# Kernel tuning notes

Measured on AMD Instinct MI355X. Metric: run time of the kernel, lower is better.

Reference implementation:

```python
import jax, jax.numpy as jnp
import numpy as np

N = 8192      # nodes
D = 256       # feature dim
GAMMA = 10.0
EPS = 1e-6
DIAG_FILL = -1e-6
# std = 0 in DGM.__init__ default -> the normal(mean=0, std=0) noise is exactly zero, so it is omitted.


def _embed(x, W, edges):
    # minimal message-passing embed_f: h = relu(xW + sum_{(s,d) in E} (xW)[s] -> d)
    h = x @ W
    agg = jax.ops.segment_sum(h[edges[0]], edges[1], num_segments=N)
    return jax.nn.relu(h + agg)


def _cdist(x):
    # pairwise euclidean distance, [N, N]
    sq = jnp.sum(x * x, axis=-1)
    d2 = sq[:, None] + sq[None, :] - 2.0 * (x @ x.T)
    return jnp.sqrt(jnp.clip(d2, 0.0))


def _layernorm(z, gamma, beta):
    # scalar-affine LayerNorm with unbiased std (torch x.std default ddof=1)
    mean = jnp.mean(z, axis=-1, keepdims=True)
    std = jnp.std(z, axis=-1, ddof=1, keepdims=True)
    return gamma * (z - mean) / (std + EPS) + beta


def _entmax15(z):
    # 1.5-entmax over last axis (Peters et al. 2019, exact sort-based algorithm)
    z = z / 2.0
    z = z - jnp.max(z, axis=-1, keepdims=True)
    zs = -jnp.sort(-z, axis=-1)                      # descending sort per row
    k = jnp.arange(1, z.shape[-1] + 1, dtype=z.dtype)
    mean = jnp.cumsum(zs, axis=-1) / k
    meansq = jnp.cumsum(zs * zs, axis=-1) / k
    ss = k * (meansq - mean * mean)
    delta = (1.0 - ss) / k
    tau = mean - jnp.sqrt(jnp.clip(delta, 0.0))
    support = jnp.sum(tau <= zs, axis=-1)            # support size per row
    tau_star = jnp.take_along_axis(tau, (support - 1)[..., None], axis=-1)
    p = jnp.clip(z - tau_star, 0.0)
    return p * p


def setup_inputs() -> dict:
    key = jax.random.key(0)
    k1, k2, k3 = jax.random.split(key, 3)
    x = jax.random.normal(k1, (N, D), dtype=jnp.float32)
    edges = jax.random.randint(k2, (2, 262144), 0, N)
    W = jax.random.normal(k3, (D, D), dtype=jnp.float32) * (1.0 / np.sqrt(D))
    gamma = jnp.full((1,), GAMMA, dtype=jnp.float32)
    beta = jnp.zeros((1,), dtype=jnp.float32)
    return {"x": x, "W": W, "gamma": gamma, "beta": beta, "edges": edges}


def reference(x, W, gamma, beta, edges):
    h = _embed(x, W, edges)                          # [N, D]
    probs = -_cdist(h)                               # [N, N]
    zn = _layernorm(probs, gamma, beta)
    idx = jnp.arange(N)
    zn = zn.at[idx, idx].set(DIAG_FILL)              # fill_diagonal_(-1e-6)
    vprobs = _entmax15(zn)                           # [N, N]
    res = (((vprobs + vprobs.T) * 0.5) > 0).astype(jnp.int32)
    logprobs = jnp.sum(res, axis=1)
    # NOTE: torch returns res.nonzero().t_() (data-dependent shape); we return the
    # equivalent dense adjacency `res` to stay jit-compatible.
    return h, res, logprobs
```

## Files before the change

### kernel.cpp

```cpp
#include <hip/hip_runtime.h>

#define N_NODES 8192
#define NMASK 8191
#define DIMF 256
#define LN_EPS 1e-6f
#define DIAG_Z (-5e-7f)
#define QSCALE 256.0f
#define QINV (1.0f / 256.0f)
#define BK 16

typedef float f32x4 __attribute__((ext_vector_type(4)));
typedef unsigned short ushort8v __attribute__((ext_vector_type(8)));

__device__ __forceinline__ unsigned short f2bf(float f) {
  unsigned int u = __float_as_uint(f);
  u = (u + 0x7FFFu + ((u >> 16) & 1u)) >> 16;
  return (unsigned short)u;
}
__device__ __forceinline__ float bf2f(unsigned short s) {
  return __uint_as_float(((unsigned int)s) << 16);
}

__global__ void DGM_22857815949798_kernel() {}

__global__ void DGM_22857815949798_dtp(const unsigned short* __restrict__ W16, int hint,
                                       int* __restrict__ flag) {
  if (blockIdx.x == 0 && threadIdx.x == 0) {
    if (hint == 0 || hint == 1) { flag[0] = hint; return; }
    float m = 0.f;
    for (int i = 0; i < 2048; ++i) {
      float v = fabsf(bf2f(W16[i]));
      if (!(v < 1e6f)) v = 1e6f;
      m += v;
    }
    flag[0] = (m * (1.0f / 2048.0f) < 10.0f) ? 1 : 0;
  }
}

__global__ __launch_bounds__(256) void DGM_22857815949798_init(int* deg, int* cursor) {
  int i = blockIdx.x * 256 + threadIdx.x;
  if (i < N_NODES) { deg[i] = 0; cursor[i] = 0; }
}

__global__ __launch_bounds__(256) void DGM_22857815949798_e1(const void* __restrict__ xv,
                                                             const void* __restrict__ Wv,
                                                             const int* __restrict__ flag,
                                                             float* __restrict__ h0) {
  __shared__ float xs[4][DIMF];
  const int bf = *flag;
  const int t = threadIdx.x;
  const int r0 = blockIdx.x * 4;
#pragma unroll
  for (int r = 0; r < 4; ++r) {
    size_t idx = (size_t)(r0 + r) * DIMF + t;
    xs[r][t] = bf ? bf2f(((const unsigned short*)xv)[idx]) : ((const float*)xv)[idx];
  }
  __syncthreads();
  float a0 = 0.f, a1 = 0.f, a2 = 0.f, a3 = 0.f;
  for (int k = 0; k < DIMF; ++k) {
    size_t wi = (size_t)k * DIMF + t;
    float w = bf ? bf2f(((const unsigned short*)Wv)[wi]) : ((const float*)Wv)[wi];
    a0 = fmaf(xs[0][k], w, a0);
    a1 = fmaf(xs[1][k], w, a1);
    a2 = fmaf(xs[2][k], w, a2);
    a3 = fmaf(xs[3][k], w, a3);
  }
  h0[(size_t)(r0 + 0) * DIMF + t] = a0;
  h0[(size_t)(r0 + 1) * DIMF + t] = a1;
  h0[(size_t)(r0 + 2) * DIMF + t] = a2;
  h0[(size_t)(r0 + 3) * DIMF + t] = a3;
}

__global__ __launch_bounds__(256) void DGM_22857815949798_deg(const int* __restrict__ dst,
                                                              int* __restrict__ deg, int E) {
  int e = blockIdx.x * 256 + threadIdx.x;
  if (e < E) atomicAdd(&deg[dst[e] & NMASK], 1);
}

__global__ __launch_bounds__(256) void DGM_22857815949798_scan(const int* __restrict__ deg,
                                                               int* __restrict__ off) {
  __shared__ int part[256];
  const int t = threadIdx.x;
  const int base = t * 32;
  int loc[32];
  int s = 0;
#pragma unroll
  for (int q = 0; q < 32; ++q) { loc[q] = s; s += deg[base + q]; }
  part[t] = s;
  __syncthreads();
  for (int o = 1; o < 256; o <<= 1) {
    int v = (t >= o) ? part[t - o] : 0;
    __syncthreads();
    part[t] += v;
    __syncthreads();
  }
  int excl = (t == 0) ? 0 : part[t - 1];
#pragma unroll
  for (int q = 0; q < 32; ++q) off[base + q] = excl + loc[q];
  if (t == 255) off[N_NODES] = excl + s;
}

__global__ __launch_bounds__(256) void DGM_22857815949798_scatter(const int* __restrict__ src,
                                                                  const int* __restrict__ dst,
                                                                  const int* __restrict__ off,
                                                                  int* __restrict__ cursor,
                                                                  int* __restrict__ adj, int E) {
  int e = blockIdx.x * 256 + threadIdx.x;
  if (e < E) {
    int d = dst[e] & NMASK;
    int p = atomicAdd(&cursor[d], 1);
    unsigned w = (unsigned)(off[d] + p);
    if (w < (unsigned)E) adj[w] = src[e] & NMASK;
  }
}

__global__ __launch_bounds__(256) void DGM_22857815949798_embed(const float* __restrict__ h0,
                                                                const int* __restrict__ adj,
                                                                const int* __restrict__ off,
                                                                void* __restrict__ hout, int outf,
                                                                float* __restrict__ sq) {
  __shared__ float rbuf[4];
  const int d = blockIdx.x;
  const int c = threadIdx.x;
  const int lane = c & 63, wv = c >> 6;
  int beg = off[d], end = off[d + 1];
  if (beg < 0) beg = 0;
  if (end > 262144) end = 262144;
  float v = h0[(size_t)d * DIMF + c];
  for (int e = beg; e < end; ++e) {
    int s = adj[e] & NMASK;
    v += h0[(size_t)s * DIMF + c];
  }
  v = fmaxf(v, 0.f);
  size_t idx = (size_t)d * DIMF + c;
  float vb;
  if (outf) { ((float*)hout)[idx] = v; vb = v; }
  else { unsigned short us = f2bf(v); ((unsigned short*)hout)[idx] = us; vb = bf2f(us); }
  float p = vb * vb;
#pragma unroll
  for (int o = 32; o; o >>= 1) p += __shfl_down(p, o);
  if (lane == 0) rbuf[wv] = p;
  __syncthreads();
  if (c == 0) sq[d] = rbuf[0] + rbuf[1] + rbuf[2] + rbuf[3];
}

__global__ __launch_bounds__(256) void DGM_22857815949798_gram(const void* __restrict__ Hv,
                                                               const float* __restrict__ sq,
                                                               void* __restrict__ Dv, int outf) {
  __shared__ float Al[BK][128];
  __shared__ float Bl[BK][128];
  __shared__ float sqi[128], sqj[128];
  const int t = threadIdx.x;

  const int bt = blockIdx.x;
  int bi = (int)((129.0f - sqrtf(129.0f * 129.0f - 8.0f * (float)bt)) * 0.5f);
  if (bi < 0) bi = 0;
  if (bi > 63) bi = 63;
  while (bi * (129 - bi) / 2 > bt) --bi;
  while ((bi + 1) * (128 - bi) / 2 <= bt) ++bi;
  const int bj = bi + (bt - bi * (129 - bi) / 2);
  const int i0 = bi * 128, j0 = bj * 128;

  const int srow = t >> 1;
  const int skh = (t & 1) * 8;
  const size_t aoff = (size_t)(i0 + srow) * DIMF + skh;
  const size_t boff = (size_t)(j0 + srow) * DIMF + skh;

  if (t < 128) sqi[t] = sq[i0 + t];
  else sqj[t - 128] = sq[j0 + t - 128];

  const int tx = t & 15, ty = t >> 4;
  float acc[8][8] = {};

  for (int ko = 0; ko < DIMF / BK; ++ko) {
    float a8[8], b8[8];
    if (outf) {
      const float* gA = (const float*)Hv + aoff + ko * BK;
      const float* gB = (const float*)Hv + boff + ko * BK;
      f32x4 x0 = *(const f32x4*)gA, x1 = *(const f32x4*)(gA + 4);
      f32x4 y0 = *(const f32x4*)gB, y1 = *(const f32x4*)(gB + 4);
#pragma unroll
      for (int q = 0; q < 4; ++q) { a8[q] = x0[q]; a8[q + 4] = x1[q]; b8[q] = y0[q]; b8[q + 4] = y1[q]; }
    } else {
      ushort8v av = *(const ushort8v*)((const unsigned short*)Hv + aoff + ko * BK);
      ushort8v bv = *(const ushort8v*)((const unsigned short*)Hv + boff + ko * BK);
#pragma unroll
      for (int q = 0; q < 8; ++q) { a8[q] = bf2f(av[q]); b8[q] = bf2f(bv[q]); }
    }
    __syncthreads();
#pragma unroll
    for (int q = 0; q < 8; ++q) {
      Al[skh + q][srow] = a8[q];
      Bl[skh + q][srow] = b8[q];
    }
    __syncthreads();
#pragma unroll
    for (int kk = 0; kk < BK; ++kk) {
      f32x4 a0 = *(const f32x4*)(&Al[kk][ty * 8]);
      f32x4 a1 = *(const f32x4*)(&Al[kk][ty * 8 + 4]);
      f32x4 b0 = *(const f32x4*)(&Bl[kk][tx * 8]);
      f32x4 b1 = *(const f32x4*)(&Bl[kk][tx * 8 + 4]);
#pragma unroll
      for (int r = 0; r < 8; ++r) {
        float ar = (r < 4) ? a0[r] : a1[r - 4];
#pragma unroll
        for (int c = 0; c < 4; ++c) {
          acc[r][c] = fmaf(ar, b0[c], acc[r][c]);
          acc[r][c + 4] = fmaf(ar, b1[c], acc[r][c + 4]);
        }
      }
    }
  }

#pragma unroll
  for (int r = 0; r < 8; ++r) {
    const int gi = i0 + ty * 8 + r;
    const float si = sqi[ty * 8 + r];
    float ddv[8];
#pragma unroll
    for (int c = 0; c < 8; ++c) {
      const int gj = j0 + tx * 8 + c;
      float d2 = si + sqj[tx * 8 + c] - 2.0f * acc[r][c];
      ddv[c] = (gi == gj) ? 0.0f : sqrtf(fmaxf(d2, 0.0f));
    }
    size_t go = (size_t)gi * N_NODES + (j0 + tx * 8);
    if (outf) {
      f32x4 o0, o1;
#pragma unroll
      for (int c = 0; c < 4; ++c) { o0[c] = ddv[c]; o1[c] = ddv[c + 4]; }
      *(f32x4*)((float*)Dv + go) = o0;
      *(f32x4*)((float*)Dv + go + 4) = o1;
    } else {
      ushort8v ov;
#pragma unroll
      for (int c = 0; c < 8; ++c) {
        int u = (int)(ddv[c] * QSCALE + 0.5f);
        ov[c] = (unsigned short)((u > 65535) ? 65535 : u);
      }
      *(ushort8v*)((unsigned short*)Dv + go) = ov;
    }
  }
  if (bi != bj) {
#pragma unroll
    for (int c = 0; c < 8; ++c) {
      const int gj = j0 + tx * 8 + c;
      const float sj = sqj[tx * 8 + c];
      float ddv[8];
#pragma unroll
      for (int r = 0; r < 8; ++r) {
        float d2 = sqi[ty * 8 + r] + sj - 2.0f * acc[r][c];
        ddv[r] = sqrtf(fmaxf(d2, 0.0f));
      }
      size_t go = (size_t)gj * N_NODES + (i0 + ty * 8);
      if (outf) {
        f32x4 o0, o1;
#pragma unroll
        for (int r = 0; r < 4; ++r) { o0[r] = ddv[r]; o1[r] = ddv[r + 4]; }
        *(f32x4*)((float*)Dv + go) = o0;
        *(f32x4*)((float*)Dv + go + 4) = o1;
      } else {
        ushort8v ov;
#pragma unroll
        for (int r = 0; r < 8; ++r) {
          int u = (int)(ddv[r] * QSCALE + 0.5f);
          ov[r] = (unsigned short)((u > 65535) ? 65535 : u);
        }
        *(ushort8v*)((unsigned short*)Dv + go) = ov;
      }
    }
  }
}

__global__ __launch_bounds__(256) void DGM_22857815949798_tau(const void* __restrict__ Dv, int outf,
                                                              const void* __restrict__ gv,
                                                              const void* __restrict__ bv,
                                                              const int* __restrict__ flag,
                                                              float* __restrict__ dthr,
                                                              float* __restrict__ taug) {
  __shared__ float cand[N_NODES];
  __shared__ int ccount;
  __shared__ float redS[4], redM[4];
  __shared__ float bc[4];
  const int i = blockIdx.x;
  const int t = threadIdx.x;
  const int lane = t & 63, wv = t >> 6;

  float dv[32];
  float sum = 0.f, dmin = 1e30f;
#pragma unroll
  for (int q = 0; q < 4; ++q) {
    const int j0 = q * 2048 + t * 8;
    const size_t go = (size_t)i * N_NODES + j0;
    if (outf) {
      f32x4 p0 = *(const f32x4*)((const float*)Dv + go);
      f32x4 p1 = *(const f32x4*)((const float*)Dv + go + 4);
#pragma unroll
      for (int e = 0; e < 8; ++e) dv[q * 8 + e] = (e < 4) ? p0[e] : p1[e - 4];
    } else {
      ushort8v pk = *(const ushort8v*)((const unsigned short*)Dv + go);
#pragma unroll
      for (int e = 0; e < 8; ++e) dv[q * 8 + e] = (float)pk[e] * QINV;
    }
#pragma unroll
    for (int e = 0; e < 8; ++e) {
      float d = dv[q * 8 + e];
      sum += d;
      if (j0 + e != i) dmin = fminf(dmin, d);
    }
  }
#pragma unroll
  for (int o = 32; o; o >>= 1) {
    sum += __shfl_down(sum, o);
    dmin = fminf(dmin, __shfl_down(dmin, o));
  }
  if (lane == 0) { redS[wv] = sum; redM[wv] = dmin; }
  __syncthreads();
  if (t == 0) {
    float S = redS[0] + redS[1] + redS[2] + redS[3];
    bc[0] = S * (1.0f / (float)N_NODES);
    bc[1] = fminf(fminf(redM[0], redM[1]), fminf(redM[2], redM[3]));
  }
  __syncthreads();
  const float mean = bc[0];
  float ss = 0.f;
#pragma unroll
  for (int q = 0; q < 32; ++q) { float u = dv[q] - mean; ss += u * u; }
#pragma unroll
  for (int o = 32; o; o >>= 1) ss += __shfl_down(ss, o);
  if (lane == 0) redS[wv] = ss;
  __syncthreads();
  if (t == 0) {
    float Q = redS[0] + redS[1] + redS[2] + redS[3];
    float sd = sqrtf(fmaxf(Q * (1.0f / (float)(N_NODES - 1)), 0.f));
    int bf = *flag;
    float gamma = bf ? bf2f(((const unsigned short*)gv)[0]) : ((const float*)gv)[0];
    float beta = bf ? bf2f(((const unsigned short*)bv)[0]) : ((const float*)bv)[0];
    float a = gamma / (2.0f * (sd + LN_EPS));
    float hb = 0.5f * beta;
    float zmax = fmaxf(a * (mean - bc[1]) + hb, DIAG_Z);
    bc[1] = a; bc[2] = zmax; bc[3] = hb;
    ccount = 0;
  }
  __syncthreads();
  const float a = bc[1], zmax = bc[2], hb = bc[3];
  const float zlo = zmax - 1.0f;
#pragma unroll
  for (int q = 0; q < 4; ++q) {
#pragma unroll
    for (int e = 0; e < 8; ++e) {
      const int j = q * 2048 + t * 8 + e;
      float z = a * (mean - dv[q * 8 + e]) + hb;
      if (j == i) z = DIAG_Z;
      if (z > zlo) {
        int p = atomicAdd(&ccount, 1);
        if (p < N_NODES) cand[p] = z;
      }
    }
  }
  __syncthreads();
  if (wv == 0) {
    const int n = (ccount < N_NODES) ? ccount : N_NODES;
    float lo = zlo, hi = zmax;
    for (int it = 0; it < 30; ++it) {
      float mid = 0.5f * (lo + hi);
      float s = 0.f;
      for (int p = lane; p < n; p += 64) {
        float u = cand[p] - mid;
        s += (u > 0.f) ? u * u : 0.f;
      }
#pragma unroll
      for (int o = 32; o; o >>= 1) s += __shfl_down(s, o);
      s = __shfl(s, 0);
      if (s > 1.f) lo = mid; else hi = mid;
    }
    if (lane == 0) {
      float tau = 0.5f * (lo + hi);
      taug[i] = tau;
      dthr[i] = mean - (tau - hb) / a;
    }
  }
}

__global__ __launch_bounds__(256) void DGM_22857815949798_res(void* __restrict__ Dv, int outf,
                                                              const float* __restrict__ dthr,
                                                              const float* __restrict__ taug,
                                                              void* __restrict__ lp) {
  __shared__ int redc[4];
  const int i = blockIdx.x;
  const int t = threadIdx.x;
  const int lane = t & 63, wv = t >> 6;
  const float di = dthr[i];
  const float ti = taug[i];
  int c = 0;
#pragma unroll
  for (int q = 0; q < 4; ++q) {
    const int j0 = q * 2048 + t * 8;
    const size_t go = (size_t)i * N_NODES + j0;
    float dvv[8];
    if (outf) {
      f32x4 p0 = *(const f32x4*)((const float*)Dv + go);
      f32x4 p1 = *(const f32x4*)((const float*)Dv + go + 4);
#pragma unroll
      for (int e = 0; e < 8; ++e) dvv[e] = (e < 4) ? p0[e] : p1[e - 4];
    } else {
      ushort8v pk = *(const ushort8v*)((const unsigned short*)Dv + go);
#pragma unroll
      for (int e = 0; e < 8; ++e) dvv[e] = (float)pk[e] * QINV;
    }
    f32x4 c0 = *(const f32x4*)(dthr + j0);
    f32x4 c1 = *(const f32x4*)(dthr + j0 + 4);
    bool rr[8];
#pragma unroll
    for (int e = 0; e < 8; ++e) {
      float dj = (e < 4) ? c0[e] : c1[e - 4];
      bool r = (dvv[e] < di) || (dvv[e] < dj);
      if (j0 + e == i) r = (DIAG_Z > ti);
      rr[e] = r;
      c += r ? 1 : 0;
    }
    if (outf) {
      f32x4 o0, o1;
#pragma unroll
      for (int e = 0; e < 4; ++e) { o0[e] = rr[e] ? 1.0f : 0.0f; o1[e] = rr[e + 4] ? 1.0f : 0.0f; }
      *(f32x4*)((float*)Dv + go) = o0;
      *(f32x4*)((float*)Dv + go + 4) = o1;
    } else {
      ushort8v ob;
#pragma unroll
      for (int e = 0; e < 8; ++e) ob[e] = rr[e] ? (unsigned short)0x3F80 : (unsigned short)0;
      *(ushort8v*)((unsigned short*)Dv + go) = ob;
    }
  }
#pragma unroll
  for (int o = 32; o; o >>= 1) c += __shfl_down(c, o);
  if (lane == 0) redc[wv] = c;
  __syncthreads();
  if (t == 0) {
    int tot = redc[0] + redc[1] + redc[2] + redc[3];
    if (outf) ((float*)lp)[i] = (float)tot;
    else ((unsigned short*)lp)[i] = f2bf((float)tot);
  }
}

static bool DGM_rng(const void* p, void** start, size_t* sz) {
  void* st = nullptr;
  size_t s = 0;
  if (hipPointerGetAttribute(&st, HIP_POINTER_ATTRIBUTE_RANGE_START_ADDR,
                             (hipDeviceptr_t)p) != hipSuccess) return false;
  if (hipPointerGetAttribute(&s, HIP_POINTER_ATTRIBUTE_RANGE_SIZE,
                             (hipDeviceptr_t)p) != hipSuccess) return false;
  *start = st; *sz = s;
  return true;
}
static bool DGM_exactish(size_t s, size_t x) { return s >= x && s < x + (size_t)(2u << 20); }

extern "C" int kernel_launch(void* const* d_in, const int* in_sizes, int n_in,
                             void* d_out, int out_size, void* d_ws, size_t ws_size,
                             hipStream_t stream) {
  (void)n_in; (void)out_size; (void)ws_size;

  int curdev = 0;
  (void)hipGetDevice(&curdev);
  int tgtdev = curdev;
  hipPointerAttribute_t pa;
  if (hipPointerGetAttributes(&pa, d_out) == hipSuccess) {
    if (pa.device >= 0 && pa.device < 64) tgtdev = pa.device;
  }
  if (tgtdev != curdev) (void)hipSetDevice(tgtdev);

  hipStreamCaptureStatus cap = hipStreamCaptureStatusNone;
  hipError_t se = hipStreamIsCapturing(stream, &cap);
  const bool validStream = (se == hipSuccess);
  const bool capturing = validStream && (cap != hipStreamCaptureStatusNone);
  hipStream_t s = validStream ? stream : (hipStream_t)0;

  const size_t OUT_B16 = 134238208ull;
  const size_t OUT_B32 = 268476416ull;
  void* outp = d_out;
  void* wsp = d_ws;
  int outf = 0;
  {
    void* st3 = nullptr; size_t s3 = 0; bool ok3 = DGM_rng(d_out, &st3, &s3);
    void* st5 = nullptr; size_t s5 = 0; bool ok5 = DGM_rng(d_ws, &st5, &s5);
    if (ok3 && st3 == d_out && DGM_exactish(s3, OUT_B16)) { outp = d_out; wsp = d_ws; outf = 0; }
    else if (ok3 && st3 == d_out && DGM_exactish(s3, OUT_B32)) { outp = d_out; wsp = d_ws; outf = 1; }
    else if (ok5 && st5 == d_ws && DGM_exactish(s5, OUT_B16)) { outp = d_ws; wsp = d_out; outf = 0; }
    else if (ok5 && st5 == d_ws && DGM_exactish(s5, OUT_B32)) { outp = d_ws; wsp = d_out; outf = 1; }
    else if (ok3 && s3 >= (200u << 20)) { outf = 1; }
  }

  int hint = -1;
  {
    void* stx = nullptr; size_t sx = 0;
    if (DGM_rng(d_in[0], &stx, &sx) && stx == d_in[0]) {
      if (DGM_exactish(sx, 4194304ull)) hint = 1;
      else if (DGM_exactish(sx, 8388608ull)) hint = 0;
    }
  }

  int E = in_sizes[4] / 2;
  if (E <= 0 || E > 8388608) E = 262144;
  const int* edges = (const int*)d_in[4];
  const int* esrc = edges;
  const int* edst = edges + E;

  const size_t esz = outf ? 4 : 2;
  char* ob = (char*)outp;
  void* h_area = ob;
  void* res_area = ob + (size_t)N_NODES * DIMF * esz;
  void* lp_area = ob + ((size_t)N_NODES * DIMF + (size_t)N_NODES * N_NODES) * esz;

  char* R = (char*)res_area;
  float* h0 = (float*)R;
  int* adj = (int*)(R + 8u * 1024 * 1024);
  int* deg = (int*)(R + 9u * 1024 * 1024);
  int* cursor = (int*)(R + 9u * 1024 * 1024 + 32768);
  int* off = (int*)(R + 9u * 1024 * 1024 + 65536);

  int* flag = (int*)wsp;
  float* sq = (float*)((char*)wsp + 4096);
  float* dthr = (float*)((char*)wsp + 4096 + 32768);
  float* taug = (float*)((char*)wsp + 4096 + 65536);

  (void)hipGetLastError();

  DGM_22857815949798_dtp<<<1, 64, 0, s>>>((const unsigned short*)d_in[1], hint, flag);
  DGM_22857815949798_init<<<N_NODES / 256, 256, 0, s>>>(deg, cursor);
  DGM_22857815949798_e1<<<N_NODES / 4, 256, 0, s>>>(d_in[0], d_in[1], flag, h0);
  DGM_22857815949798_deg<<<(E + 255) / 256, 256, 0, s>>>(edst, deg, E);
  DGM_22857815949798_scan<<<1, 256, 0, s>>>(deg, off);
  DGM_22857815949798_scatter<<<(E + 255) / 256, 256, 0, s>>>(esrc, edst, off, cursor, adj, E);
  DGM_22857815949798_embed<<<N_NODES, 256, 0, s>>>(h0, adj, off, h_area, outf, sq);
  DGM_22857815949798_gram<<<2080, 256, 0, s>>>(h_area, sq, res_area, outf);
  DGM_22857815949798_tau<<<N_NODES, 256, 0, s>>>(res_area, outf, d_in[2], d_in[3], flag, dthr, taug);
  DGM_22857815949798_res<<<N_NODES, 256, 0, s>>>(res_area, outf, dthr, taug, lp_area);

  hipError_t err = hipGetLastError();
  if (!capturing) {
    if (err != hipSuccess) {
      (void)hipDeviceSynchronize();
      (void)hipGetLastError();
    }
    (void)hipStreamSynchronize(s);
  }

  if (tgtdev != curdev) (void)hipSetDevice(curdev);
  return 0;
}

extern "C" int launch(void* const* a, const int* b, int c, void* d, int e, void* f,
                      size_t g, hipStream_t h) { return kernel_launch(a, b, c, d, e, f, g, h); }
extern "C" int run(void* const* a, const int* b, int c, void* d, int e, void* f,
                   size_t g, hipStream_t h) { return kernel_launch(a, b, c, d, e, f, g, h); }
extern "C" int kernel_main(void* const* a, const int* b, int c, void* d, int e, void* f,
                           size_t g, hipStream_t h) { return kernel_launch(a, b, c, d, e, f, g, h); }
extern "C" int DGM_22857815949798(void* const* a, const int* b, int c, void* d, int e, void* f,
                                  size_t g, hipStream_t h) { return kernel_launch(a, b, c, d, e, f, g, h); }
```

Measured before the change: 797.6 us.

## Use bf16 MFMA gram kernel for distance matrix in bf16 output path

Adds a new gram kernel that computes the pairwise dot products with bf16 MFMA 16x16x32 instructions on 128x128 tiles, staged through padded LDS. It writes quantized 16-bit distances through an LDS buffer so the global stores are coalesced. It runs on the full grid instead of the upper-triangle grid, so it does twice the tile count but replaces the scalar fp32 inner loop. The W magnitude probe is also parallelized across 256 threads with a wavefront reduction. The new kernel is only used when the output is not fp32.

```diff
diff --git a/kernel.cpp b/kernel.cpp
--- a/kernel.cpp
+++ b/kernel.cpp
@@ -8,9 +8,11 @@
 #define QSCALE 256.0f
 #define QINV (1.0f / 256.0f)
 #define BK 16
+#define LDA 40
 
 typedef float f32x4 __attribute__((ext_vector_type(4)));
 typedef unsigned short ushort8v __attribute__((ext_vector_type(8)));
+typedef short short8v __attribute__((ext_vector_type(8)));
 
 __device__ __forceinline__ unsigned short f2bf(float f) {
   unsigned int u = __float_as_uint(f);
@@ -23,18 +25,22 @@
 
 __global__ void DGM_22857815949798_kernel() {}
 
-__global__ void DGM_22857815949798_dtp(const unsigned short* __restrict__ W16, int hint,
-                                       int* __restrict__ flag) {
-  if (blockIdx.x == 0 && threadIdx.x == 0) {
-    if (hint == 0 || hint == 1) { flag[0] = hint; return; }
-    float m = 0.f;
-    for (int i = 0; i < 2048; ++i) {
-      float v = fabsf(bf2f(W16[i]));
-      if (!(v < 1e6f)) v = 1e6f;
-      m += v;
-    }
-    flag[0] = (m * (1.0f / 2048.0f) < 10.0f) ? 1 : 0;
-  }
+__global__ __launch_bounds__(256) void DGM_22857815949798_dtp(const unsigned short* __restrict__ W16,
+                                                              int hint, int* __restrict__ flag) {
+  __shared__ float red[4];
+  const int t = threadIdx.x;
+  if (hint == 0 || hint == 1) { if (t == 0) flag[0] = hint; return; }
+  float m = 0.f;
+  for (int i = t; i < 2048; i += 256) {
+    float v = fabsf(bf2f(W16[i]));
+    if (!(v < 1e6f)) v = 1e6f;
+    m += v;
+  }
+#pragma unroll
+  for (int o = 32; o; o >>= 1) m += __shfl_down(m, o);
+  if ((t & 63) == 0) red[t >> 6] = m;
+  __syncthreads();
+  if (t == 0) flag[0] = ((red[0] + red[1] + red[2] + red[3]) * (1.0f / 2048.0f) < 10.0f) ? 1 : 0;
 }
 
 __global__ __launch_bounds__(256) void DGM_22857815949798_init(int* deg, int* cursor) {
@@ -144,6 +150,82 @@
   if (c == 0) sq[d] = rbuf[0] + rbuf[1] + rbuf[2] + rbuf[3];
 }
 
+__global__ __launch_bounds__(256) void DGM_22857815949798_gramm(const unsigned short* __restrict__ H,
+                                                                const float* __restrict__ sq,
+                                                                unsigned short* __restrict__ dq) {
+  __shared__ __align__(16) unsigned short lds[16384];
+  unsigned short* Alds = lds;
+  unsigned short* Blds = lds + 128 * LDA;
+  const int t = threadIdx.x;
+  const int lane = t & 63, wv = t >> 6;
+  const int i0 = blockIdx.y * 128, j0 = blockIdx.x * 128;
+  const int wM = (wv >> 1) * 64, wN = (wv & 1) * 64;
+  const int quad = lane >> 4, cid = lane & 15;
+  const int arow = t >> 2;
+  const int kcol = (t & 3) * 8;
+
+  const unsigned short* gA = H + (size_t)(i0 + arow) * DIMF + kcol;
+  const unsigned short* gB = H + (size_t)(j0 + arow) * DIMF + kcol;
+
+  f32x4 acc[4][4] = {};
+
+  for (int ko = 0; ko < 8; ++ko) {
+    const int kk = ko * 32;
+    ushort8v a0 = *(const ushort8v*)(gA + kk);
+    ushort8v a1 = *(const ushort8v*)(gA + (size_t)64 * DIMF + kk);
+    ushort8v b0 = *(const ushort8v*)(gB + kk);
+    ushort8v b1 = *(const ushort8v*)(gB + (size_t)64 * DIMF + kk);
+    __syncthreads();
+    *(ushort8v*)(Alds + arow * LDA + kcol) = a0;
+    *(ushort8v*)(Alds + (arow + 64) * LDA + kcol) = a1;
+    *(ushort8v*)(Blds + arow * LDA + kcol) = b0;
+    *(ushort8v*)(Blds + (arow + 64) * LDA + kcol) = b1;
+    __syncthreads();
+
+    short8v af[4], bq[4];
+#pragma unroll
+    for (int mi = 0; mi < 4; ++mi)
+      af[mi] = *(const short8v*)(Alds + (wM + mi * 16 + cid) * LDA + quad * 8);
+#pragma unroll
+    for (int ni = 0; ni < 4; ++ni)
+      bq[ni] = *(const short8v*)(Blds + (wN + ni * 16 + cid) * LDA + quad * 8);
+#pragma unroll
+    for (int mi = 0; mi < 4; ++mi)
+#pragma unroll
+      for (int ni = 0; ni < 4; ++ni)
+        acc[mi][ni] = __builtin_amdgcn_mfma_f32_16x16x32_bf16(af[mi], bq[ni], acc[mi][ni], 0, 0, 0);
+  }
+  __syncthreads();
+
+  unsigned short* wbuf = lds + wv * 4096;
+#pragma unroll
+  for (int mi = 0; mi < 4; ++mi) {
+#pragma unroll
+    for (int r = 0; r < 4; ++r) {
+      const int lrow = mi * 16 + quad * 4 + r;
+      const int gi = i0 + wM + lrow;
+      const float si = sq[gi];
+#pragma unroll
+      for (int ni = 0; ni < 4; ++ni) {
+        const int gj = j0 + wN + ni * 16 + cid;
+        float d2 = si + sq[gj] - 2.0f * acc[mi][ni][r];
+        float dd = (gi == gj) ? 0.0f : sqrtf(fmaxf(d2, 0.0f));
+        int u = (int)(dd * QSCALE + 0.5f);
+        u = (u > 65535) ? 65535 : u;
+        wbuf[lrow * 64 + ni * 16 + cid] = (unsigned short)u;
+      }
+    }
+  }
+#pragma unroll
+  for (int it = 0; it < 8; ++it) {
+    int o = it * 512 + lane * 8;
+    int row = o >> 6;
+    int col = o & 63;
+    size_t goff = (size_t)(i0 + wM + row) * N_NODES + (size_t)(j0 + wN + col);
+    *(ushort8v*)(dq + goff) = *(const ushort8v*)(wbuf + o);
+  }
+}
+
 __global__ __launch_bounds__(256) void DGM_22857815949798_gram(const void* __restrict__ Hv,
                                                                const float* __restrict__ sq,
                                                                void* __restrict__ Dv, int outf) {
@@ -524,14 +606,20 @@
 
   (void)hipGetLastError();
 
-  DGM_22857815949798_dtp<<<1, 64, 0, s>>>((const unsigned short*)d_in[1], hint, flag);
+  DGM_22857815949798_dtp<<<1, 256, 0, s>>>((const unsigned short*)d_in[1], hint, flag);
   DGM_22857815949798_init<<<N_NODES / 256, 256, 0, s>>>(deg, cursor);
   DGM_22857815949798_e1<<<N_NODES / 4, 256, 0, s>>>(d_in[0], d_in[1], flag, h0);
   DGM_22857815949798_deg<<<(E + 255) / 256, 256, 0, s>>>(edst, deg, E);
   DGM_22857815949798_scan<<<1, 256, 0, s>>>(deg, off);
   DGM_22857815949798_scatter<<<(E + 255) / 256, 256, 0, s>>>(esrc, edst, off, cursor, adj, E);
   DGM_22857815949798_embed<<<N_NODES, 256, 0, s>>>(h0, adj, off, h_area, outf, sq);
-  DGM_22857815949798_gram<<<2080, 256, 0, s>>>(h_area, sq, res_area, outf);
+  if (outf) {
+    DGM_22857815949798_gram<<<2080, 256, 0, s>>>(h_area, sq, res_area, outf);
+  } else {
+    dim3 gg(N_NODES / 128, N_NODES / 128);
+    DGM_22857815949798_gramm<<<gg, 256, 0, s>>>((const unsigned short*)h_area, sq,
+                                                (unsigned short*)res_area);
+  }
   DGM_22857815949798_tau<<<N_NODES, 256, 0, s>>>(res_area, outf, d_in[2], d_in[3], flag, dthr, taug);
   DGM_22857815949798_res<<<N_NODES, 256, 0, s>>>(res_area, outf, dthr, taug, lp_area);
 
```

Result: faster. 764.5 us (-4.1%).
